# Kernel tuning notes

Hardware: AMD Instinct MI355X
Metric: run time of the kernel (lower is better)

## Reference

```python
import jax, jax.numpy as jnp
import numpy as np
import math

B, S, D, H, TD = 256, 200, 64, 512, 8


def setup_inputs():
    key = jax.random.key(0)
    ks = jax.random.split(key, 12)
    sd, sh, so = 1.0 / math.sqrt(D), 1.0 / math.sqrt(H), 1.0 / math.sqrt(H + TD)
    return dict(
        x=jax.random.normal(ks[0], (B, S, D), jnp.float32),
        a=jax.random.normal(ks[3], (B, TD), jnp.float32),
        t=jnp.cumsum(jax.random.uniform(ks[2], (B, S), jnp.float32), axis=1),
        mask=(jax.random.uniform(ks[1], (B, S, D)) < 0.8).astype(jnp.float32),
        w_dg_x=jax.random.normal(ks[4], (D,), jnp.float32) * sd,
        b_dg_x=jnp.zeros((D,), jnp.float32),
        W_dg_h=jax.random.normal(ks[5], (H, D), jnp.float32) * sd,
        b_dg_h=jnp.zeros((H,), jnp.float32),
        W=jax.random.normal(ks[6], (3 * H, D), jnp.float32) * sd,
        U=jax.random.normal(ks[7], (3 * H, H), jnp.float32) * sh,
        V=jax.random.normal(ks[8], (3 * H, D), jnp.float32) * sd,
        b=jnp.zeros((3 * H,), jnp.float32),
        attn_v=jnp.ones((H,), jnp.float32),
        W_out=jax.random.normal(ks[9], (H, H + TD), jnp.float32) * so,
        b_out=jnp.zeros((H,), jnp.float32),
    )


def reference(x, a, t, mask, w_dg_x, b_dg_x, W_dg_h, b_dg_h, W, U, V, b, attn_v, W_out, b_out):
    # ---- GRU-D preprocessing: per-feature time gaps delta ----
    x_tm = jnp.transpose(x, (1, 0, 2))    # (S,B,D) time-major
    m_tm = jnp.transpose(mask, (1, 0, 2))
    dt = jnp.diff(t, axis=1, prepend=t[:, :1])      # (B,S), dt[0]=0
    dt_tm = jnp.transpose(dt)[:, :, None]           # (S,B,1)
    # delta[i] = dt[i] + (1 - mask[i-1]) * delta[i-1]; ones at step 0 -> delta[0]=0
    m_prev = jnp.concatenate([jnp.ones((1,) + m_tm.shape[1:], m_tm.dtype), m_tm[:-1]], axis=0)

    def delta_step(d, inp):
        dt_i, mp_i = inp
        d = dt_i + (1.0 - mp_i) * d
        return d, d

    _, delta_tm = jax.lax.scan(delta_step, jnp.zeros((B, D), x.dtype), (dt_tm, m_prev))

    # empirical mean of observed values for imputation
    x_mean = (mask * x).sum((0, 1)) / jnp.maximum(mask.sum((0, 1)), 1.0)  # (D,)

    Wz, Wr, Wh = W[:H], W[H:2 * H], W[2 * H:]
    Uz, Ur, Uh = U[:H], U[H:2 * H], U[2 * H:]
    Vz, Vr, Vh = V[:H], V[H:2 * H], V[2 * H:]
    bz, br, bh = b[:H], b[H:2 * H], b[2 * H:]

    def cell(carry, inp):
        h, x_last = carry
        x_i, m_i, d_i = inp                                        # (B,D) each
        gamma_x = jnp.exp(-jax.nn.relu(w_dg_x * d_i + b_dg_x))     # (B,D) input decay
        gamma_h = jnp.exp(-jax.nn.relu(d_i @ W_dg_h.T + b_dg_h))   # (B,H) hidden decay
        x_hat = m_i * x_i + (1.0 - m_i) * (gamma_x * x_last + (1.0 - gamma_x) * x_mean)
        h_dec = gamma_h * h
        z = jax.nn.sigmoid(x_hat @ Wz.T + h_dec @ Uz.T + m_i @ Vz.T + bz)
        r = jax.nn.sigmoid(x_hat @ Wr.T + h_dec @ Ur.T + m_i @ Vr.T + br)
        h_til = jnp.tanh(x_hat @ Wh.T + (r * h_dec) @ Uh.T + m_i @ Vh.T + bh)
        h_new = (1.0 - z) * h_dec + z * h_til
        x_last_new = m_i * x_i + (1.0 - m_i) * x_last
        return (h_new, x_last_new), h_new

    init = (jnp.zeros((B, H), x.dtype), jnp.zeros((B, D), x.dtype))
    _, h_all = jax.lax.scan(cell, init, (x_tm, m_tm, delta_tm))    # (S,B,H)

    # ---- attention pooling over time (softmax along seq dim, as in torch dim=0) ----
    score = (h_all @ attn_v) / math.sqrt(H)        # (S,B)
    w_attn = jax.nn.softmax(score, axis=0)
    attn_h = (h_all * w_attn[..., None]).sum(0)    # (B,H)

    # ---- treatment head ----
    return jnp.concatenate([attn_h, a], axis=1) @ W_out.T + b_out  # (B,H)
```

## Files before the change

### kernel.cpp

```cpp
#include <hip/hip_runtime.h>
#include <hip/hip_bf16.h>
#include <stdint.h>


typedef unsigned short u16;
typedef unsigned int   u32;
typedef unsigned long long u64;
typedef short bfrag  __attribute__((ext_vector_type(8)));
typedef u16   u16x8  __attribute__((ext_vector_type(8)));
typedef float f32x4  __attribute__((ext_vector_type(4)));

#define NB 256
#define NS 200
#define ND 64
#define NH 512

#define MFMA(a,b,c) __builtin_amdgcn_mfma_f32_16x16x32_bf16((a),(b),(c),0,0,0)

union UQ { u16x8 h; bfrag s; u64 u[2]; uint4 q; };

__device__ __forceinline__ float b2f(u16 v){ union { float f; u32 u; } c; c.u = ((u32)v) << 16; return c.f; }
__device__ __forceinline__ u16 f2b(float f){ union { float f; u32 u; } c; c.f = f; u32 r = c.u + 0x7FFFu + ((c.u >> 16) & 1u); return (u16)(r >> 16); }
__device__ __forceinline__ float sigm(float x){ return 1.f / (1.f + __expf(-x)); }
__device__ __forceinline__ float tanh_f(float x){ return 1.f - 2.f / (1.f + __expf(2.f * x)); }

__device__ __forceinline__ u64 cload64(const void* p){
  return __hip_atomic_load((const u64*)p, __ATOMIC_RELAXED, __HIP_MEMORY_SCOPE_AGENT);
}
__device__ __forceinline__ void cstore64(void* p, u64 v){
  __hip_atomic_store((u64*)p, v, __ATOMIC_RELAXED, __HIP_MEMORY_SCOPE_AGENT);
}
__device__ __forceinline__ u32 cload32(const u32* p){
  return __hip_atomic_load(p, __ATOMIC_RELAXED, __HIP_MEMORY_SCOPE_AGENT);
}
__device__ __forceinline__ void cstore32(u32* p, u32 v){
  __hip_atomic_store(p, v, __ATOMIC_RELAXED, __HIP_MEMORY_SCOPE_AGENT);
}
__device__ __forceinline__ bool poll_ge(const u32* wp, u32 tgt){
  int fuel = 1 << 20;
  while (true) {
    u32 v = cload32(wp);
    if (__all(v >= tgt)) return true;
    if (--fuel == 0) return false;
  }
}
__device__ __forceinline__ bfrag ldfrag(const float* src){
  f32x4 lo = *(const f32x4*)src;
  f32x4 hi = *(const f32x4*)(src + 4);
  UQ z;
  z.h[0]=f2b(lo[0]); z.h[1]=f2b(lo[1]); z.h[2]=f2b(lo[2]); z.h[3]=f2b(lo[3]);
  z.h[4]=f2b(hi[0]); z.h[5]=f2b(hi[1]); z.h[6]=f2b(hi[2]); z.h[7]=f2b(hi[3]);
  return z.s;
}
__device__ __forceinline__ const float* wsrc(const float* Um, const float* Wm,
                                             const float* Vm, int c, int k0){
  if (k0 < 512) return Um + (size_t)c * 512 + k0;
  if (k0 < 576) return Wm + (size_t)c * 64 + (k0 - 512);
  return Vm + (size_t)c * 64 + (k0 - 576);
}


__global__ void transpose_k(const float* __restrict__ Wout, float* __restrict__ WT){
  int i = blockIdx.x * 256 + threadIdx.x;
  if (i < 520 * 512) { int k = i >> 9, ho = i & 511; WT[i] = Wout[ho * 520 + k]; }
}

__global__ void mean1_k(const float* __restrict__ x, const float* __restrict__ mask,
                        float* __restrict__ PX, float* __restrict__ PM){
  int s = blockIdx.x, tid = threadIdx.x;
  __shared__ float lx[256], lm[256];
  float xa = 0.f, ma = 0.f;
  for (int i = tid; i < NB * ND; i += 256) {
    int b = i >> 6, d = i & 63;
    size_t ix = ((size_t)b * NS + s) * 64 + d;
    float m = mask[ix];
    xa += m * x[ix]; ma += m;
  }
  lx[tid] = xa; lm[tid] = ma;
  __syncthreads();
  if (tid < 64) {
    PX[(size_t)s * 64 + tid] = lx[tid] + lx[tid + 64] + lx[tid + 128] + lx[tid + 192];
    PM[(size_t)s * 64 + tid] = lm[tid] + lm[tid + 64] + lm[tid + 128] + lm[tid + 192];
  }
}

__global__ void mean2_k(const float* __restrict__ PX, const float* __restrict__ PM,
                        float* __restrict__ XMEAN){
  int d = threadIdx.x;
  float sx = 0.f, sm = 0.f;
  for (int s = 0; s < NS; ++s){ sx += PX[s * 64 + d]; sm += PM[s * 64 + d]; }
  XMEAN[d] = sx / fmaxf(sm, 1.f);
}

__global__ void prep_k(const float* __restrict__ x, const float* __restrict__ mask,
                       const float* __restrict__ tc, const float* __restrict__ wdgx,
                       const float* __restrict__ bdgx, const float* __restrict__ XMEAN,
                       u16* __restrict__ XHAT, u16* __restrict__ MASKB, u16* __restrict__ DELTA){
  int g = blockIdx.x * 256 + threadIdx.x;
  int b = g >> 6, d = g & 63;
  float xmean = XMEAN[d], wx = wdgx[d], bx = bdgx[d];
  float xl = 0.f, del = 0.f, tprev = 0.f, mprev = 1.f;
  for (int s = 0; s < NS; ++s){
    float tv = tc[b * NS + s];
    float dtv = (s == 0) ? 0.f : (tv - tprev);
    tprev = tv;
    del = dtv + (1.f - mprev) * del;
    size_t ix = ((size_t)b * NS + s) * 64 + d;
    float m = mask[ix], xv = x[ix];
    float gx = __expf(-fmaxf(0.f, wx * del + bx));
    float xh = m * xv + (1.f - m) * (gx * xl + (1.f - gx) * xmean);
    size_t ox = ((size_t)s * NB + b) * 64 + d;
    XHAT[ox] = f2b(xh); MASKB[ox] = f2b(m); DELTA[ox] = f2b(del);
    xl = m * xv + (1.f - m) * xl;
    mprev = m;
  }
}

__global__ __launch_bounds__(256, 1) void grud_rnn(
    const float* __restrict__ Um, const float* __restrict__ Wm, const float* __restrict__ Vm,
    const float* __restrict__ bv, const float* __restrict__ Wdg, const float* __restrict__ bdg,
    const u16* __restrict__ XHAT, const u16* __restrict__ MASKB, const u16* __restrict__ DELTA,
    u16* __restrict__ HDECB, u16* __restrict__ RHB, u16* __restrict__ ZZB,
    u16* __restrict__ GAMB, u16* __restrict__ HALL, u32* __restrict__ flags)
{
  const int tid = threadIdx.x, lane = tid & 63, wid = tid >> 6, bid = blockIdx.x;
  const int rb = bid / 9, role = bid % 9, m0 = rb * 16;
  const int l16 = lane & 15, krow = lane >> 4;
  const int r4 = lane >> 2, cb = (lane & 3) * 8;
  u32* FB = flags + rb * 64;

  __shared__ u16 panel[80 * 16 * 8];
  __shared__ float xb[4][16 * 34];
  __shared__ int s_ab;
  float* xw = xb[wid];
  const f32x4 Z4 = {0.f, 0.f, 0.f, 0.f};
  if (tid == 0) s_ab = 0;
  __syncthreads();

  if (role < 4) {
    const int pw = role * 4 + wid;
    const int cw = role * 128 + wid * 32;
    bfrag BR[20][2], BH[20][2];
    #pragma unroll
    for (int kk = 0; kk < 20; ++kk) {
      const int k0 = kk * 32 + krow * 8;
      #pragma unroll
      for (int t2 = 0; t2 < 2; ++t2) {
        BR[kk][t2] = ldfrag(wsrc(Um, Wm, Vm, 512  + cw + t2 * 16 + l16, k0));
        BH[kk][t2] = ldfrag(wsrc(Um, Wm, Vm, 1024 + cw + t2 * 16 + l16, k0));
      }
    }
    const float br0 = bv[512 + cw + l16],  br1 = bv[512 + cw + 16 + l16];
    const float bh0 = bv[1024 + cw + l16], bh1 = bv[1024 + cw + 16 + l16];

    for (int t = 0; t < NS; ++t) {
      { const int kbx = tid >> 4, row = tid & 15;
        const u16* sp = (kbx < 8 ? XHAT : MASKB) + ((size_t)t * NB + m0 + row) * 64 + (kbx & 7) * 8;
        *(uint4*)&panel[((64 + kbx) * 16 + row) * 8] = *(const uint4*)sp; }
      if (wid == 0) {
        const u32* wp; u32 tgt;
        if (lane < 16)      { wp = FB + lane; tgt = (u32)t; }
        else if (lane == 16){ wp = FB + 48; tgt = (u32)((t + 1 < NS) ? (t + 1) : (NS - 1)); }
        else                { wp = FB; tgt = 0u; }
        if (!poll_ge(wp, tgt)) s_ab = 1;
      }
      __syncthreads();
      if (s_ab) break;
      u64 gm0 = 0, gm1 = 0;
      if (t + 1 < NS) {
        const u16* gpb = GAMB + (((size_t)((t + 1) & 1) * 16 + rb) * 16 + r4) * 512 + cw + cb;
        gm0 = cload64(gpb); gm1 = cload64(gpb + 4);
      }
      { const int row = tid >> 4, sc = (tid & 15) * 32;
        u16* dp = &panel[((sc >> 3) * 16 + row) * 8];
        if (t > 0) {
          const u16* hs = HDECB + (size_t)(m0 + row) * 512 + sc;
          u64 a0 = cload64(hs),      a1 = cload64(hs + 4),  a2 = cload64(hs + 8),  a3 = cload64(hs + 12);
          u64 a4 = cload64(hs + 16), a5 = cload64(hs + 20), a6 = cload64(hs + 24), a7 = cload64(hs + 28);
          *(u64*)(dp)       = a0; *(u64*)(dp + 4)   = a1;
          *(u64*)(dp + 128) = a2; *(u64*)(dp + 132) = a3;
          *(u64*)(dp + 256) = a4; *(u64*)(dp + 260) = a5;
          *(u64*)(dp + 384) = a6; *(u64*)(dp + 388) = a7;
        } else {
          *(u64*)(dp)       = 0; *(u64*)(dp + 4)   = 0;
          *(u64*)(dp + 128) = 0; *(u64*)(dp + 132) = 0;
          *(u64*)(dp + 256) = 0; *(u64*)(dp + 260) = 0;
          *(u64*)(dp + 384) = 0; *(u64*)(dp + 388) = 0;
        }
      }
      __syncthreads();
      f32x4 a0 = {br0, br0, br0, br0}, a1 = {br1, br1, br1, br1};
      #pragma unroll
      for (int kk = 0; kk < 20; ++kk) {
        bfrag a = *(const bfrag*)&panel[((kk * 4 + krow) * 16 + l16) * 8];
        a0 = MFMA(a, BR[kk][0], a0); a1 = MFMA(a, BR[kk][1], a1);
      }
      #pragma unroll
      for (int j = 0; j < 4; ++j) {
        xw[(krow * 4 + j) * 34 + l16] = a0[j];
        xw[(krow * 4 + j) * 34 + 16 + l16] = a1[j];
      }
      UQ hd_; hd_.h = *(const u16x8*)&panel[(((cw + cb) >> 3) * 16 + r4) * 8];
      UQ rh_;
      #pragma unroll
      for (int q = 0; q < 8; ++q) {
        float rv = sigm(xw[r4 * 34 + cb + q]);
        rh_.h[q] = f2b(rv * b2f(hd_.h[q]));
      }
      u16* rdst = RHB + (size_t)(m0 + r4) * 512 + cw + cb;
      cstore64(rdst, rh_.u[0]); cstore64(rdst + 4, rh_.u[1]);
      asm volatile("s_waitcnt vmcnt(0)" ::: "memory");
      if (lane == 0) cstore32(FB + 16 + pw, (u32)(t + 1));
      if (wid == 0) {
        const u32* wp; u32 tgt;
        if (lane < 16)      { wp = FB + 16 + lane; tgt = (u32)(t + 1); }
        else if (lane < 32) { wp = FB + 32 + (lane - 16); tgt = (u32)(t + 1); }
        else                { wp = FB; tgt = 0u; }
        if (!poll_ge(wp, tgt)) s_ab = 1;
      }
      __syncthreads();
      if (s_ab) break;
      { const int row = tid >> 4, sc = (tid & 15) * 32;
        const u16* rs = RHB + (size_t)(m0 + row) * 512 + sc;
        u64 a0_ = cload64(rs),      a1_ = cload64(rs + 4),  a2_ = cload64(rs + 8),  a3_ = cload64(rs + 12);
        u64 a4_ = cload64(rs + 16), a5_ = cload64(rs + 20), a6_ = cload64(rs + 24), a7_ = cload64(rs + 28);
        u16* dp = &panel[((sc >> 3) * 16 + row) * 8];
        *(u64*)(dp)       = a0_; *(u64*)(dp + 4)   = a1_;
        *(u64*)(dp + 128) = a2_; *(u64*)(dp + 132) = a3_;
        *(u64*)(dp + 256) = a4_; *(u64*)(dp + 260) = a5_;
        *(u64*)(dp + 384) = a6_; *(u64*)(dp + 388) = a7_;
      }
      __syncthreads();
      u64 zz0 = cload64(ZZB + (size_t)(m0 + r4) * 512 + cw + cb);
      u64 zz1 = cload64(ZZB + (size_t)(m0 + r4) * 512 + cw + cb + 4);
      f32x4 h0_ = {bh0, bh0, bh0, bh0}, h1_ = {bh1, bh1, bh1, bh1};
      #pragma unroll
      for (int kk = 0; kk < 20; ++kk) {
        bfrag a = *(const bfrag*)&panel[((kk * 4 + krow) * 16 + l16) * 8];
        h0_ = MFMA(a, BH[kk][0], h0_); h1_ = MFMA(a, BH[kk][1], h1_);
      }
      #pragma unroll
      for (int j = 0; j < 4; ++j) {
        xw[(krow * 4 + j) * 34 + l16] = h0_[j];
        xw[(krow * 4 + j) * 34 + 16 + l16] = h1_[j];
      }
      UQ zz_; zz_.u[0] = zz0; zz_.u[1] = zz1;
      UQ gm_; gm_.u[0] = gm0; gm_.u[1] = gm1;
      UQ hw_, hdn_;
      #pragma unroll
      for (int q = 0; q < 8; ++q) {
        float til = tanh_f(xw[r4 * 34 + cb + q]);
        float z = b2f(zz_.h[q]);
        float hn = (1.f - z) * b2f(hd_.h[q]) + z * til;
        hw_.h[q] = f2b(hn);
        hdn_.h[q] = f2b(b2f(gm_.h[q]) * hn);
      }
      if (t + 1 < NS) {
        u16* hdst = HDECB + (size_t)(m0 + r4) * 512 + cw + cb;
        cstore64(hdst, hdn_.u[0]); cstore64(hdst + 4, hdn_.u[1]);
      }
      asm volatile("s_waitcnt vmcnt(0)" ::: "memory");
      if (lane == 0) cstore32(FB + 0 + pw, (u32)(t + 1));
      u16* hp = HALL + ((size_t)t * NB + m0 + r4) * 512 + cw + cb;
      *(u64*)hp = hw_.u[0]; *(u64*)(hp + 4) = hw_.u[1];
      __syncthreads();
    }
  } else if (role < 8) {
    const int pw = (role - 4) * 4 + wid;
    const int cw = (role - 4) * 128 + wid * 32;
    bfrag BZ[20][2];
    #pragma unroll
    for (int kk = 0; kk < 20; ++kk) {
      const int k0 = kk * 32 + krow * 8;
      #pragma unroll
      for (int t2 = 0; t2 < 2; ++t2)
        BZ[kk][t2] = ldfrag(wsrc(Um, Wm, Vm, cw + t2 * 16 + l16, k0));
    }
    const float bz0 = bv[cw + l16], bz1 = bv[cw + 16 + l16];

    for (int t = 0; t < NS; ++t) {
      { const int kbx = tid >> 4, row = tid & 15;
        const u16* sp = (kbx < 8 ? XHAT : MASKB) + ((size_t)t * NB + m0 + row) * 64 + (kbx & 7) * 8;
        *(uint4*)&panel[((64 + kbx) * 16 + row) * 8] = *(const uint4*)sp; }
      if (wid == 0) {
        const u32* wp = (lane < 16) ? (FB + lane) : FB;
        u32 tgt = (lane < 16) ? (u32)t : 0u;
        if (!poll_ge(wp, tgt)) s_ab = 1;
      }
      __syncthreads();
      if (s_ab) break;
      { const int row = tid >> 4, sc = (tid & 15) * 32;
        u16* dp = &panel[((sc >> 3) * 16 + row) * 8];
        if (t > 0) {
          const u16* hs = HDECB + (size_t)(m0 + row) * 512 + sc;
          u64 a0 = cload64(hs),      a1 = cload64(hs + 4),  a2 = cload64(hs + 8),  a3 = cload64(hs + 12);
          u64 a4 = cload64(hs + 16), a5 = cload64(hs + 20), a6 = cload64(hs + 24), a7 = cload64(hs + 28);
          *(u64*)(dp)       = a0; *(u64*)(dp + 4)   = a1;
          *(u64*)(dp + 128) = a2; *(u64*)(dp + 132) = a3;
          *(u64*)(dp + 256) = a4; *(u64*)(dp + 260) = a5;
          *(u64*)(dp + 384) = a6; *(u64*)(dp + 388) = a7;
        } else {
          *(u64*)(dp)       = 0; *(u64*)(dp + 4)   = 0;
          *(u64*)(dp + 128) = 0; *(u64*)(dp + 132) = 0;
          *(u64*)(dp + 256) = 0; *(u64*)(dp + 260) = 0;
          *(u64*)(dp + 384) = 0; *(u64*)(dp + 388) = 0;
        }
      }
      __syncthreads();
      f32x4 a0 = {bz0, bz0, bz0, bz0}, a1 = {bz1, bz1, bz1, bz1};
      #pragma unroll
      for (int kk = 0; kk < 20; ++kk) {
        bfrag a = *(const bfrag*)&panel[((kk * 4 + krow) * 16 + l16) * 8];
        a0 = MFMA(a, BZ[kk][0], a0); a1 = MFMA(a, BZ[kk][1], a1);
      }
      #pragma unroll
      for (int j = 0; j < 4; ++j) {
        xw[(krow * 4 + j) * 34 + l16] = a0[j];
        xw[(krow * 4 + j) * 34 + 16 + l16] = a1[j];
      }
      UQ zq;
      #pragma unroll
      for (int q = 0; q < 8; ++q) zq.h[q] = f2b(sigm(xw[r4 * 34 + cb + q]));
      u16* zdst = ZZB + (size_t)(m0 + r4) * 512 + cw + cb;
      cstore64(zdst, zq.u[0]); cstore64(zdst + 4, zq.u[1]);
      asm volatile("s_waitcnt vmcnt(0)" ::: "memory");
      if (lane == 0) cstore32(FB + 32 + pw, (u32)(t + 1));
      __syncthreads();
    }
  } else {
    bfrag BG[8][2];
    #pragma unroll
    for (int ct = 0; ct < 8; ++ct)
      #pragma unroll
      for (int kx = 0; kx < 2; ++kx)
        BG[ct][kx] = ldfrag(Wdg + (size_t)(wid * 128 + ct * 16 + l16) * 64 + kx * 32 + krow * 8);
    float gb4[4][8];
    #pragma unroll
    for (int grp = 0; grp < 4; ++grp)
      #pragma unroll
      for (int q = 0; q < 8; ++q) gb4[grp][q] = bdg[wid * 128 + grp * 32 + cb + q];

    for (int tt = 1; tt < NS; ++tt) {
      if (wid == 0) {
        const u32* wp = (lane < 16) ? (FB + lane) : FB;
        u32 tgt = (lane < 16 && tt >= 3) ? (u32)(tt - 2) : 0u;
        if (!poll_ge(wp, tgt)) s_ab = 1;
      }
      if (tid < 128) {
        const int kb = tid >> 4, row = tid & 15;
        const u16* sp = DELTA + ((size_t)tt * NB + m0 + row) * 64 + kb * 8;
        *(uint4*)&panel[(kb * 16 + row) * 8] = *(const uint4*)sp;
      }
      __syncthreads();
      if (s_ab) break;
      u16* orow_ = GAMB + (((size_t)(tt & 1) * 16 + rb) * 16 + r4) * 512 + wid * 128;
      #pragma unroll
      for (int grp = 0; grp < 4; ++grp) {
        f32x4 ac0 = Z4, ac1 = Z4;
        #pragma unroll
        for (int kx = 0; kx < 2; ++kx) {
          bfrag a = *(const bfrag*)&panel[((kx * 4 + krow) * 16 + l16) * 8];
          ac0 = MFMA(a, BG[grp*2][kx], ac0); ac1 = MFMA(a, BG[grp*2+1][kx], ac1);
        }
        #pragma unroll
        for (int j = 0; j < 4; ++j) { xw[(krow*4+j)*34 + l16] = ac0[j]; xw[(krow*4+j)*34 + 16 + l16] = ac1[j]; }
        UQ ov;
        #pragma unroll
        for (int q = 0; q < 8; ++q)
          ov.h[q] = f2b(__expf(-fmaxf(0.f, xw[r4 * 34 + cb + q] + gb4[grp][q])));
        cstore64(orow_ + grp * 32 + cb, ov.u[0]); cstore64(orow_ + grp * 32 + cb + 4, ov.u[1]);
      }
      asm volatile("s_waitcnt vmcnt(0)" ::: "memory");
      __syncthreads();
      if (tid == 0) cstore32(FB + 48, (u32)tt);
    }
  }
}


__global__ void attn_k(const u16* __restrict__ HALL, const float* __restrict__ av,
                       float* __restrict__ ATTN){
  const int b = blockIdx.x, tid = threadIdx.x, lane = tid & 63, wid = tid >> 6;
  __shared__ float avs[512], wgt[256], red[8];
  for (int i = tid; i < 512; i += 256) avs[i] = av[i];
  __syncthreads();
  float val = -3.0e38f;
  if (tid < NS) {
    const u16* hp = HALL + ((size_t)tid * NB + b) * 512;
    float acc = 0.f;
    for (int h = 0; h < 512; h += 8) {
      UQ w; w.q = *(const uint4*)(hp + h);
      #pragma unroll
      for (int j = 0; j < 8; ++j) acc += b2f(w.h[j]) * avs[h + j];
    }
    val = acc * 0.04419417382415922f;
  }
  float m = val;
  #pragma unroll
  for (int off = 32; off; off >>= 1) m = fmaxf(m, __shfl_xor(m, off, 64));
  if (lane == 0) red[wid] = m;
  __syncthreads();
  m = fmaxf(fmaxf(red[0], red[1]), fmaxf(red[2], red[3]));
  float e = (tid < NS) ? __expf(val - m) : 0.f;
  float sum = e;
  #pragma unroll
  for (int off = 32; off; off >>= 1) sum += __shfl_xor(sum, off, 64);
  if (lane == 0) red[4 + wid] = sum;
  __syncthreads();
  const float ssum = red[4] + red[5] + red[6] + red[7];
  wgt[tid] = e / ssum;
  __syncthreads();
  float a0 = 0.f, a1 = 0.f;
  const int h0 = tid * 2;
  for (int s = 0; s < NS; ++s) {
    float w = wgt[s];
    u32 pr = *(const u32*)(HALL + ((size_t)s * NB + b) * 512 + h0);
    a0 += w * b2f((u16)(pr & 0xFFFFu));
    a1 += w * b2f((u16)(pr >> 16));
  }
  ATTN[(size_t)b * 512 + h0] = a0;
  ATTN[(size_t)b * 512 + h0 + 1] = a1;
}

__global__ void out_k(const float* __restrict__ ATTN, const float* __restrict__ Ain,
                      const float* __restrict__ WT, const float* __restrict__ bout,
                      float* __restrict__ OUT){
  const int g = blockIdx.x, tid = threadIdx.x;
  __shared__ float ah[4][520];
  for (int i = tid; i < 4 * 520; i += 256) {
    int bb = i / 520, k = i % 520;
    int b = g * 4 + bb;
    ah[bb][k] = (k < 512) ? ATTN[(size_t)b * 512 + k] : Ain[b * 8 + (k - 512)];
  }
  __syncthreads();
  #pragma unroll
  for (int part = 0; part < 2; ++part) {
    const int ho = part * 256 + tid;
    float a0 = bout[ho], a1 = a0, a2 = a0, a3 = a0;
    for (int k = 0; k < 520; ++k) {
      float w = WT[(size_t)k * 512 + ho];
      a0 += ah[0][k] * w; a1 += ah[1][k] * w; a2 += ah[2][k] * w; a3 += ah[3][k] * w;
    }
    OUT[(size_t)(g * 4 + 0) * 512 + ho] = a0;
    OUT[(size_t)(g * 4 + 1) * 512 + ho] = a1;
    OUT[(size_t)(g * 4 + 2) * 512 + ho] = a2;
    OUT[(size_t)(g * 4 + 3) * 512 + ho] = a3;
  }
}


extern "C" void kernel_launch(void* const* d_in, const int* in_sizes, int n_in,
                              void* d_out, int out_size, void* d_ws, size_t ws_size,
                              hipStream_t stream) {
  (void)in_sizes; (void)n_in; (void)out_size; (void)ws_size;
  const float* x    = (const float*)d_in[0];
  const float* a_in = (const float*)d_in[1];
  const float* tc   = (const float*)d_in[2];
  const float* mask = (const float*)d_in[3];
  const float* wdgx = (const float*)d_in[4];
  const float* bdgx = (const float*)d_in[5];
  const float* Wdgh = (const float*)d_in[6];
  const float* bdgh = (const float*)d_in[7];
  const float* Wm   = (const float*)d_in[8];
  const float* Um   = (const float*)d_in[9];
  const float* Vm   = (const float*)d_in[10];
  const float* bvv  = (const float*)d_in[11];
  const float* attv = (const float*)d_in[12];
  const float* Wout = (const float*)d_in[13];
  const float* bout = (const float*)d_in[14];

  char* ws = (char*)d_ws;
  size_t o = 0;
  auto al = [&](size_t sz) { size_t r = o; o += (sz + 255) & ~(size_t)255; return r; };
  u32*   flags = (u32*)  (ws + al(16 * 64 * 4));
  float* XMEAN = (float*)(ws + al(256));
  float* PX    = (float*)(ws + al((size_t)NS * 64 * 4));
  float* PM    = (float*)(ws + al((size_t)NS * 64 * 4));
  u16*   XHAT  = (u16*)  (ws + al((size_t)NS * NB * 64 * 2));
  u16*   MASKB = (u16*)  (ws + al((size_t)NS * NB * 64 * 2));
  u16*   DELTA = (u16*)  (ws + al((size_t)NS * NB * 64 * 2));
  u16*   HDECB = (u16*)  (ws + al((size_t)NB * NH * 2));
  u16*   RHB   = (u16*)  (ws + al((size_t)NB * NH * 2));
  u16*   ZZB   = (u16*)  (ws + al((size_t)NB * NH * 2));
  u16*   GAMB  = (u16*)  (ws + al((size_t)2 * 16 * 16 * 512 * 2));
  u16*   HALL  = (u16*)  (ws + al((size_t)NS * NB * NH * 2));
  float* ATTN  = (float*)(ws + al((size_t)NB * NH * 4));
  float* WT    = (float*)(ws + al((size_t)520 * 512 * 4));

  hipMemsetAsync(flags, 0, 16 * 64 * 4, stream);

  transpose_k<<<(520 * 512 + 255) / 256, 256, 0, stream>>>(Wout, WT);
  mean1_k<<<NS, 256, 0, stream>>>(x, mask, PX, PM);
  mean2_k<<<1, 64, 0, stream>>>(PX, PM, XMEAN);
  prep_k<<<NB * ND / 256, 256, 0, stream>>>(x, mask, tc, wdgx, bdgx, XMEAN, XHAT, MASKB, DELTA);
  grud_rnn<<<144, 256, 0, stream>>>(Um, Wm, Vm, bvv, Wdgh, bdgh, XHAT, MASKB, DELTA,
                                    HDECB, RHB, ZZB, GAMB, HALL, flags);
  attn_k<<<NB, 256, 0, stream>>>(HALL, attv, ATTN);
  out_k<<<64, 256, 0, stream>>>(ATTN, a_in, WT, bout, (float*)d_out);
}
```

Measured before the change: 2.026 ms.

## Interleave two row-blocks per workgroup in persistent GRU-D recurrent kernel

Each persistent workgroup now handles two 16-row batch blocks instead of one, alternating the r-gate, z-gate, candidate and gamma phases between the two blocks. The grid is halved from 144 to 72 workgroups. While one block waits on cross-workgroup flags, the other block's matmul work can proceed, which is meant to hide synchronisation latency in the time-step recurrence. In exchange, each workgroup does twice the serial work per step, uses more LDS, and runs on fewer CUs.

```diff
diff --git a/kernel.cpp b/kernel.cpp
--- a/kernel.cpp
+++ b/kernel.cpp
@@ -57,6 +57,24 @@
   if (k0 < 512) return Um + (size_t)c * 512 + k0;
   if (k0 < 576) return Wm + (size_t)c * 64 + (k0 - 512);
   return Vm + (size_t)c * 64 + (k0 - 576);
+}
+__device__ __forceinline__ void stage_bf16(u16* dst, const u16* src, int tid, bool zero){
+  const int row = tid >> 4, sc = (tid & 15) * 32;
+  u16* dp = &dst[((sc >> 3) * 16 + row) * 8];
+  if (!zero) {
+    const u16* hs = src + (size_t)row * 512 + sc;
+    u64 a0 = cload64(hs),      a1 = cload64(hs + 4),  a2 = cload64(hs + 8),  a3 = cload64(hs + 12);
+    u64 a4 = cload64(hs + 16), a5 = cload64(hs + 20), a6 = cload64(hs + 24), a7 = cload64(hs + 28);
+    *(u64*)(dp)       = a0; *(u64*)(dp + 4)   = a1;
+    *(u64*)(dp + 128) = a2; *(u64*)(dp + 132) = a3;
+    *(u64*)(dp + 256) = a4; *(u64*)(dp + 260) = a5;
+    *(u64*)(dp + 384) = a6; *(u64*)(dp + 388) = a7;
+  } else {
+    *(u64*)(dp)       = 0; *(u64*)(dp + 4)   = 0;
+    *(u64*)(dp + 128) = 0; *(u64*)(dp + 132) = 0;
+    *(u64*)(dp + 256) = 0; *(u64*)(dp + 260) = 0;
+    *(u64*)(dp + 384) = 0; *(u64*)(dp + 388) = 0;
+  }
 }
 
 
@@ -124,18 +142,33 @@
     u16* __restrict__ GAMB, u16* __restrict__ HALL, u32* __restrict__ flags)
 {
   const int tid = threadIdx.x, lane = tid & 63, wid = tid >> 6, bid = blockIdx.x;
-  const int rb = bid / 9, role = bid % 9, m0 = rb * 16;
+  const int cl = bid / 9, role = bid % 9;
+  const int RB0 = cl * 2, RB1 = RB0 + 1;
+  const int M00 = RB0 * 16, M01 = RB1 * 16;
   const int l16 = lane & 15, krow = lane >> 4;
   const int r4 = lane >> 2, cb = (lane & 3) * 8;
-  u32* FB = flags + rb * 64;
-
-  __shared__ u16 panel[80 * 16 * 8];
+  u32* FB0 = flags + RB0 * 64;
+  u32* FB1 = flags + RB1 * 64;
+
+  __shared__ u16 panels[2][80 * 16 * 8];
   __shared__ float xb[4][16 * 34];
   __shared__ int s_ab;
+  u16* panel0 = panels[0];
+  u16* panel1 = panels[1];
   float* xw = xb[wid];
   const f32x4 Z4 = {0.f, 0.f, 0.f, 0.f};
   if (tid == 0) s_ab = 0;
   __syncthreads();
+
+  auto pollw = [&](const u32* base16, u32 tgt16, const u32* base2, u32 tgt2, int n2){
+    if (wid == 0) {
+      const u32* wp; u32 tgt;
+      if (lane < 16)           { wp = base16 + lane; tgt = tgt16; }
+      else if (lane < 16 + n2) { wp = base2 + (lane - 16); tgt = tgt2; }
+      else                     { wp = base16; tgt = 0u; }
+      if (!poll_ge(wp, tgt)) s_ab = 1;
+    }
+  };
 
   if (role < 4) {
     const int pw = role * 4 + wid;
@@ -153,116 +186,107 @@
     const float br0 = bv[512 + cw + l16],  br1 = bv[512 + cw + 16 + l16];
     const float bh0 = bv[1024 + cw + l16], bh1 = bv[1024 + cw + 16 + l16];
 
-    for (int t = 0; t < NS; ++t) {
-      { const int kbx = tid >> 4, row = tid & 15;
-        const u16* sp = (kbx < 8 ? XHAT : MASKB) + ((size_t)t * NB + m0 + row) * 64 + (kbx & 7) * 8;
-        *(uint4*)&panel[((64 + kbx) * 16 + row) * 8] = *(const uint4*)sp; }
-      if (wid == 0) {
-        const u32* wp; u32 tgt;
-        if (lane < 16)      { wp = FB + lane; tgt = (u32)t; }
-        else if (lane == 16){ wp = FB + 48; tgt = (u32)((t + 1 < NS) ? (t + 1) : (NS - 1)); }
-        else                { wp = FB; tgt = 0u; }
-        if (!poll_ge(wp, tgt)) s_ab = 1;
-      }
-      __syncthreads();
-      if (s_ab) break;
-      u64 gm0 = 0, gm1 = 0;
-      if (t + 1 < NS) {
-        const u16* gpb = GAMB + (((size_t)((t + 1) & 1) * 16 + rb) * 16 + r4) * 512 + cw + cb;
-        gm0 = cload64(gpb); gm1 = cload64(gpb + 4);
-      }
-      { const int row = tid >> 4, sc = (tid & 15) * 32;
-        u16* dp = &panel[((sc >> 3) * 16 + row) * 8];
-        if (t > 0) {
-          const u16* hs = HDECB + (size_t)(m0 + row) * 512 + sc;
-          u64 a0 = cload64(hs),      a1 = cload64(hs + 4),  a2 = cload64(hs + 8),  a3 = cload64(hs + 12);
-          u64 a4 = cload64(hs + 16), a5 = cload64(hs + 20), a6 = cload64(hs + 24), a7 = cload64(hs + 28);
-          *(u64*)(dp)       = a0; *(u64*)(dp + 4)   = a1;
-          *(u64*)(dp + 128) = a2; *(u64*)(dp + 132) = a3;
-          *(u64*)(dp + 256) = a4; *(u64*)(dp + 260) = a5;
-          *(u64*)(dp + 384) = a6; *(u64*)(dp + 388) = a7;
-        } else {
-          *(u64*)(dp)       = 0; *(u64*)(dp + 4)   = 0;
-          *(u64*)(dp + 128) = 0; *(u64*)(dp + 132) = 0;
-          *(u64*)(dp + 256) = 0; *(u64*)(dp + 260) = 0;
-          *(u64*)(dp + 384) = 0; *(u64*)(dp + 388) = 0;
-        }
-      }
-      __syncthreads();
-      f32x4 a0 = {br0, br0, br0, br0}, a1 = {br1, br1, br1, br1};
+    UQ hd0_, hd1_;
+
+    auto hop1 = [&](u16* pan, int m0x, u32* FBX, UQ& hdx, int t){
+      stage_bf16(pan, HDECB + (size_t)m0x * 512, tid, t == 0);
+      __syncthreads();
+      f32x4 A0 = {br0, br0, br0, br0}, A1 = {br1, br1, br1, br1};
       #pragma unroll
       for (int kk = 0; kk < 20; ++kk) {
-        bfrag a = *(const bfrag*)&panel[((kk * 4 + krow) * 16 + l16) * 8];
-        a0 = MFMA(a, BR[kk][0], a0); a1 = MFMA(a, BR[kk][1], a1);
+        bfrag a = *(const bfrag*)&pan[((kk * 4 + krow) * 16 + l16) * 8];
+        A0 = MFMA(a, BR[kk][0], A0); A1 = MFMA(a, BR[kk][1], A1);
       }
       #pragma unroll
       for (int j = 0; j < 4; ++j) {
-        xw[(krow * 4 + j) * 34 + l16] = a0[j];
-        xw[(krow * 4 + j) * 34 + 16 + l16] = a1[j];
-      }
-      UQ hd_; hd_.h = *(const u16x8*)&panel[(((cw + cb) >> 3) * 16 + r4) * 8];
+        xw[(krow * 4 + j) * 34 + l16] = A0[j];
+        xw[(krow * 4 + j) * 34 + 16 + l16] = A1[j];
+      }
+      hdx.h = *(const u16x8*)&pan[(((cw + cb) >> 3) * 16 + r4) * 8];
       UQ rh_;
       #pragma unroll
       for (int q = 0; q < 8; ++q) {
         float rv = sigm(xw[r4 * 34 + cb + q]);
-        rh_.h[q] = f2b(rv * b2f(hd_.h[q]));
-      }
-      u16* rdst = RHB + (size_t)(m0 + r4) * 512 + cw + cb;
+        rh_.h[q] = f2b(rv * b2f(hdx.h[q]));
+      }
+      u16* rdst = RHB + (size_t)(m0x + r4) * 512 + cw + cb;
       cstore64(rdst, rh_.u[0]); cstore64(rdst + 4, rh_.u[1]);
       asm volatile("s_waitcnt vmcnt(0)" ::: "memory");
-      if (lane == 0) cstore32(FB + 16 + pw, (u32)(t + 1));
-      if (wid == 0) {
-        const u32* wp; u32 tgt;
-        if (lane < 16)      { wp = FB + 16 + lane; tgt = (u32)(t + 1); }
-        else if (lane < 32) { wp = FB + 32 + (lane - 16); tgt = (u32)(t + 1); }
-        else                { wp = FB; tgt = 0u; }
-        if (!poll_ge(wp, tgt)) s_ab = 1;
-      }
-      __syncthreads();
-      if (s_ab) break;
-      { const int row = tid >> 4, sc = (tid & 15) * 32;
-        const u16* rs = RHB + (size_t)(m0 + row) * 512 + sc;
-        u64 a0_ = cload64(rs),      a1_ = cload64(rs + 4),  a2_ = cload64(rs + 8),  a3_ = cload64(rs + 12);
-        u64 a4_ = cload64(rs + 16), a5_ = cload64(rs + 20), a6_ = cload64(rs + 24), a7_ = cload64(rs + 28);
-        u16* dp = &panel[((sc >> 3) * 16 + row) * 8];
-        *(u64*)(dp)       = a0_; *(u64*)(dp + 4)   = a1_;
-        *(u64*)(dp + 128) = a2_; *(u64*)(dp + 132) = a3_;
-        *(u64*)(dp + 256) = a4_; *(u64*)(dp + 260) = a5_;
-        *(u64*)(dp + 384) = a6_; *(u64*)(dp + 388) = a7_;
-      }
-      __syncthreads();
-      u64 zz0 = cload64(ZZB + (size_t)(m0 + r4) * 512 + cw + cb);
-      u64 zz1 = cload64(ZZB + (size_t)(m0 + r4) * 512 + cw + cb + 4);
-      f32x4 h0_ = {bh0, bh0, bh0, bh0}, h1_ = {bh1, bh1, bh1, bh1};
+      if (lane == 0) cstore32(FBX + 16 + pw, (u32)(t + 1));
+    };
+
+    auto hop2 = [&](u16* pan, int m0x, u32* FBX, UQ& hdx, u64 gma, u64 gmb, int t){
+      stage_bf16(pan, RHB + (size_t)m0x * 512, tid, false);
+      __syncthreads();
+      u64 zz0 = cload64(ZZB + (size_t)(m0x + r4) * 512 + cw + cb);
+      u64 zz1 = cload64(ZZB + (size_t)(m0x + r4) * 512 + cw + cb + 4);
+      f32x4 H0 = {bh0, bh0, bh0, bh0}, H1 = {bh1, bh1, bh1, bh1};
       #pragma unroll
       for (int kk = 0; kk < 20; ++kk) {
-        bfrag a = *(const bfrag*)&panel[((kk * 4 + krow) * 16 + l16) * 8];
-        h0_ = MFMA(a, BH[kk][0], h0_); h1_ = MFMA(a, BH[kk][1], h1_);
+        bfrag a = *(const bfrag*)&pan[((kk * 4 + krow) * 16 + l16) * 8];
+        H0 = MFMA(a, BH[kk][0], H0); H1 = MFMA(a, BH[kk][1], H1);
       }
       #pragma unroll
       for (int j = 0; j < 4; ++j) {
-        xw[(krow * 4 + j) * 34 + l16] = h0_[j];
-        xw[(krow * 4 + j) * 34 + 16 + l16] = h1_[j];
+        xw[(krow * 4 + j) * 34 + l16] = H0[j];
+        xw[(krow * 4 + j) * 34 + 16 + l16] = H1[j];
       }
       UQ zz_; zz_.u[0] = zz0; zz_.u[1] = zz1;
-      UQ gm_; gm_.u[0] = gm0; gm_.u[1] = gm1;
+      UQ gm_; gm_.u[0] = gma; gm_.u[1] = gmb;
       UQ hw_, hdn_;
       #pragma unroll
       for (int q = 0; q < 8; ++q) {
         float til = tanh_f(xw[r4 * 34 + cb + q]);
         float z = b2f(zz_.h[q]);
-        float hn = (1.f - z) * b2f(hd_.h[q]) + z * til;
+        float hn = (1.f - z) * b2f(hdx.h[q]) + z * til;
         hw_.h[q] = f2b(hn);
         hdn_.h[q] = f2b(b2f(gm_.h[q]) * hn);
       }
       if (t + 1 < NS) {
-        u16* hdst = HDECB + (size_t)(m0 + r4) * 512 + cw + cb;
+        u16* hdst = HDECB + (size_t)(m0x + r4) * 512 + cw + cb;
         cstore64(hdst, hdn_.u[0]); cstore64(hdst + 4, hdn_.u[1]);
       }
       asm volatile("s_waitcnt vmcnt(0)" ::: "memory");
-      if (lane == 0) cstore32(FB + 0 + pw, (u32)(t + 1));
-      u16* hp = HALL + ((size_t)t * NB + m0 + r4) * 512 + cw + cb;
+      if (lane == 0) cstore32(FBX + 0 + pw, (u32)(t + 1));
+      u16* hp = HALL + ((size_t)t * NB + m0x + r4) * 512 + cw + cb;
       *(u64*)hp = hw_.u[0]; *(u64*)(hp + 4) = hw_.u[1];
+    };
+
+    for (int t = 0; t < NS; ++t) {
+      {
+        const int kbx = tid >> 4, row = tid & 15;
+        const u16* s0 = (kbx < 8 ? XHAT : MASKB) + ((size_t)t * NB + M00 + row) * 64 + (kbx & 7) * 8;
+        *(uint4*)&panel0[((64 + kbx) * 16 + row) * 8] = *(const uint4*)s0;
+        const u16* s1 = (kbx < 8 ? XHAT : MASKB) + ((size_t)t * NB + M01 + row) * 64 + (kbx & 7) * 8;
+        *(uint4*)&panel1[((64 + kbx) * 16 + row) * 8] = *(const uint4*)s1;
+      }
+      const u32 gtgt = (u32)((t + 1 < NS) ? (t + 1) : (NS - 1));
+      pollw(FB0 + 0, (u32)t, FB0 + 48, gtgt, 1);
+      __syncthreads();
+      if (s_ab) break;
+      u64 g00 = 0, g01 = 0;
+      if (t + 1 < NS) {
+        const u16* gp = GAMB + (((size_t)((t + 1) & 1) * 16 + RB0) * 16 + r4) * 512 + cw + cb;
+        g00 = cload64(gp); g01 = cload64(gp + 4);
+      }
+      hop1(panel0, M00, FB0, hd0_, t);
+      pollw(FB1 + 0, (u32)t, FB1 + 48, gtgt, 1);
+      __syncthreads();
+      if (s_ab) break;
+      u64 g10 = 0, g11 = 0;
+      if (t + 1 < NS) {
+        const u16* gp = GAMB + (((size_t)((t + 1) & 1) * 16 + RB1) * 16 + r4) * 512 + cw + cb;
+        g10 = cload64(gp); g11 = cload64(gp + 4);
+      }
+      hop1(panel1, M01, FB1, hd1_, t);
+      pollw(FB0 + 16, (u32)(t + 1), FB0 + 32, (u32)(t + 1), 16);
+      __syncthreads();
+      if (s_ab) break;
+      hop2(panel0, M00, FB0, hd0_, g00, g01, t);
+      pollw(FB1 + 16, (u32)(t + 1), FB1 + 32, (u32)(t + 1), 16);
+      __syncthreads();
+      if (s_ab) break;
+      hop2(panel1, M01, FB1, hd1_, g10, g11, t);
       __syncthreads();
     }
   } else if (role < 8) {
@@ -278,53 +302,43 @@
     }
     const float bz0 = bv[cw + l16], bz1 = bv[cw + 16 + l16];
 
+    auto zhop = [&](u16* pan, int m0x, u32* FBX, int t){
+      stage_bf16(pan, HDECB + (size_t)m0x * 512, tid, t == 0);
+      __syncthreads();
+      f32x4 A0 = {bz0, bz0, bz0, bz0}, A1 = {bz1, bz1, bz1, bz1};
+      #pragma unroll
+      for (int kk = 0; kk < 20; ++kk) {
+        bfrag a = *(const bfrag*)&pan[((kk * 4 + krow) * 16 + l16) * 8];
+        A0 = MFMA(a, BZ[kk][0], A0); A1 = MFMA(a, BZ[kk][1], A1);
+      }
+      #pragma unroll
+      for (int j = 0; j < 4; ++j) {
+        xw[(krow * 4 + j) * 34 + l16] = A0[j];
+        xw[(krow * 4 + j) * 34 + 16 + l16] = A1[j];
+      }
+      UQ zq;
+      #pragma unroll
+      for (int q = 0; q < 8; ++q) zq.h[q] = f2b(sigm(xw[r4 * 34 + cb + q]));
+      u16* zdst = ZZB + (size_t)(m0x + r4) * 512 + cw + cb;
+      cstore64(zdst, zq.u[0]); cstore64(zdst + 4, zq.u[1]);
+      asm volatile("s_waitcnt vmcnt(0)" ::: "memory");
+      if (lane == 0) cstore32(FBX + 32 + pw, (u32)(t + 1));
+    };
+
     for (int t = 0; t < NS; ++t) {
       { const int kbx = tid >> 4, row = tid & 15;
-        const u16* sp = (kbx < 8 ? XHAT : MASKB) + ((size_t)t * NB + m0 + row) * 64 + (kbx & 7) * 8;
-        *(uint4*)&panel[((64 + kbx) * 16 + row) * 8] = *(const uint4*)sp; }
-      if (wid == 0) {
-        const u32* wp = (lane < 16) ? (FB + lane) : FB;
-        u32 tgt = (lane < 16) ? (u32)t : 0u;
-        if (!poll_ge(wp, tgt)) s_ab = 1;
-      }
+        const u16* s0 = (kbx < 8 ? XHAT : MASKB) + ((size_t)t * NB + M00 + row) * 64 + (kbx & 7) * 8;
+        *(uint4*)&panel0[((64 + kbx) * 16 + row) * 8] = *(const uint4*)s0;
+        const u16* s1 = (kbx < 8 ? XHAT : MASKB) + ((size_t)t * NB + M01 + row) * 64 + (kbx & 7) * 8;
+        *(uint4*)&panel1[((64 + kbx) * 16 + row) * 8] = *(const uint4*)s1; }
+      pollw(FB0 + 0, (u32)t, FB0, 0u, 0);
       __syncthreads();
       if (s_ab) break;
-      { const int row = tid >> 4, sc = (tid & 15) * 32;
-        u16* dp = &panel[((sc >> 3) * 16 + row) * 8];
-        if (t > 0) {
-          const u16* hs = HDECB + (size_t)(m0 + row) * 512 + sc;
-          u64 a0 = cload64(hs),      a1 = cload64(hs + 4),  a2 = cload64(hs + 8),  a3 = cload64(hs + 12);
-          u64 a4 = cload64(hs + 16), a5 = cload64(hs + 20), a6 = cload64(hs + 24), a7 = cload64(hs + 28);
-          *(u64*)(dp)       = a0; *(u64*)(dp + 4)   = a1;
-          *(u64*)(dp + 128) = a2; *(u64*)(dp + 132) = a3;
-          *(u64*)(dp + 256) = a4; *(u64*)(dp + 260) = a5;
-          *(u64*)(dp + 384) = a6; *(u64*)(dp + 388) = a7;
-        } else {
-          *(u64*)(dp)       = 0; *(u64*)(dp + 4)   = 0;
-          *(u64*)(dp + 128) = 0; *(u64*)(dp + 132) = 0;
-          *(u64*)(dp + 256) = 0; *(u64*)(dp + 260) = 0;
-          *(u64*)(dp + 384) = 0; *(u64*)(dp + 388) = 0;
-        }
-      }
-      __syncthreads();
-      f32x4 a0 = {bz0, bz0, bz0, bz0}, a1 = {bz1, bz1, bz1, bz1};
-      #pragma unroll
-      for (int kk = 0; kk < 20; ++kk) {
-        bfrag a = *(const bfrag*)&panel[((kk * 4 + krow) * 16 + l16) * 8];
-        a0 = MFMA(a, BZ[kk][0], a0); a1 = MFMA(a, BZ[kk][1], a1);
-      }
-      #pragma unroll
-      for (int j = 0; j < 4; ++j) {
-        xw[(krow * 4 + j) * 34 + l16] = a0[j];
-        xw[(krow * 4 + j) * 34 + 16 + l16] = a1[j];
-      }
-      UQ zq;
-      #pragma unroll
-      for (int q = 0; q < 8; ++q) zq.h[q] = f2b(sigm(xw[r4 * 34 + cb + q]));
-      u16* zdst = ZZB + (size_t)(m0 + r4) * 512 + cw + cb;
-      cstore64(zdst, zq.u[0]); cstore64(zdst + 4, zq.u[1]);
-      asm volatile("s_waitcnt vmcnt(0)" ::: "memory");
-      if (lane == 0) cstore32(FB + 32 + pw, (u32)(t + 1));
+      zhop(panel0, M00, FB0, t);
+      pollw(FB1 + 0, (u32)t, FB1, 0u, 0);
+      __syncthreads();
+      if (s_ab) break;
+      zhop(panel1, M01, FB1, t);
       __syncthreads();
     }
   } else {
@@ -340,27 +354,27 @@
       #pragma unroll
       for (int q = 0; q < 8; ++q) gb4[grp][q] = bdg[wid * 128 + grp * 32 + cb + q];
 
-    for (int tt = 1; tt < NS; ++tt) {
+    auto ghop = [&](u16* pan, int rbx, int m0x, u32* FBX, int tt){
       if (wid == 0) {
-        const u32* wp = (lane < 16) ? (FB + lane) : FB;
+        const u32* wp = (lane < 16) ? (FBX + lane) : FBX;
         u32 tgt = (lane < 16 && tt >= 3) ? (u32)(tt - 2) : 0u;
         if (!poll_ge(wp, tgt)) s_ab = 1;
       }
       if (tid < 128) {
         const int kb = tid >> 4, row = tid & 15;
-        const u16* sp = DELTA + ((size_t)tt * NB + m0 + row) * 64 + kb * 8;
-        *(uint4*)&panel[(kb * 16 + row) * 8] = *(const uint4*)sp;
-      }
-      __syncthreads();
-      if (s_ab) break;
-      u16* orow_ = GAMB + (((size_t)(tt & 1) * 16 + rb) * 16 + r4) * 512 + wid * 128;
+        const u16* sp = DELTA + ((size_t)tt * NB + m0x + row) * 64 + kb * 8;
+        *(uint4*)&pan[(kb * 16 + row) * 8] = *(const uint4*)sp;
+      }
+      __syncthreads();
+      if (s_ab) return false;
+      u16* orow_ = GAMB + (((size_t)(tt & 1) * 16 + rbx) * 16 + r4) * 512 + wid * 128;
       #pragma unroll
       for (int grp = 0; grp < 4; ++grp) {
         f32x4 ac0 = Z4, ac1 = Z4;
         #pragma unroll
         for (int kx = 0; kx < 2; ++kx) {
-          bfrag a = *(const bfrag*)&panel[((kx * 4 + krow) * 16 + l16) * 8];
-          ac0 = MFMA(a, BG[grp*2][kx], ac0); ac1 = MFMA(a, BG[grp*2+1][kx], ac1);
+          bfrag a = *(const bfrag*)&pan[((kx * 4 + krow) * 16 + l16) * 8];
+          ac0 = MFMA(a, BG[grp * 2][kx], ac0); ac1 = MFMA(a, BG[grp * 2 + 1][kx], ac1);
         }
         #pragma unroll
         for (int j = 0; j < 4; ++j) { xw[(krow*4+j)*34 + l16] = ac0[j]; xw[(krow*4+j)*34 + 16 + l16] = ac1[j]; }
@@ -372,7 +386,13 @@
       }
       asm volatile("s_waitcnt vmcnt(0)" ::: "memory");
       __syncthreads();
-      if (tid == 0) cstore32(FB + 48, (u32)tt);
+      if (tid == 0) cstore32(FBX + 48, (u32)tt);
+      return true;
+    };
+
+    for (int tt = 1; tt < NS; ++tt) {
+      if (!ghop(panel0, RB0, M00, FB0, tt)) break;
+      if (!ghop(panel1, RB1, M01, FB1, tt)) break;
     }
   }
 }
@@ -493,8 +513,8 @@
   mean1_k<<<NS, 256, 0, stream>>>(x, mask, PX, PM);
   mean2_k<<<1, 64, 0, stream>>>(PX, PM, XMEAN);
   prep_k<<<NB * ND / 256, 256, 0, stream>>>(x, mask, tc, wdgx, bdgx, XMEAN, XHAT, MASKB, DELTA);
-  grud_rnn<<<144, 256, 0, stream>>>(Um, Wm, Vm, bvv, Wdgh, bdgh, XHAT, MASKB, DELTA,
-                                    HDECB, RHB, ZZB, GAMB, HALL, flags);
+  grud_rnn<<<72, 256, 0, stream>>>(Um, Wm, Vm, bvv, Wdgh, bdgh, XHAT, MASKB, DELTA,
+                                   HDECB, RHB, ZZB, GAMB, HALL, flags);
   attn_k<<<NB, 256, 0, stream>>>(HALL, attv, ATTN);
   out_k<<<64, 256, 0, stream>>>(ATTN, a_in, WT, bout, (float*)d_out);
 }
```

Measured after the change: 3.541 ms. 74.8% more time.
